# Kernel tuning notes

Measured on AMD Instinct MI355X. Metric: run time of the kernel, lower is better.

Reference implementation:

```python
import jax, jax.numpy as jnp
import numpy as np

EPS = 1e-6
T = 10.0
STEPS = 3
BN_EPS = 1e-5

def _normalize(x, axis):
    n = jnp.sqrt(jnp.sum(x * x, axis=axis, keepdims=True))
    return x / jnp.maximum(n, EPS)

def _vq_step(X, D):
    # X: (B, d, n), D: (B, d, r)
    Dn = _normalize(D, 1)
    Xn = _normalize(X, 1)
    cos = jnp.einsum('bdr,bdn->brn', Dn, Xn)          # (B, r, n)
    C = jax.nn.softmax(cos / T, axis=1)               # softmax over r
    XCt = jnp.einsum('bdn,brn->bdr', X, C)            # (B, d, r)
    sums = jnp.maximum(jnp.sum(C, axis=2), EPS)       # (B, r)
    D2 = _normalize(XCt / sums[:, None, :], 1)
    Xbar = jnp.einsum('bdr,brn->bdn', D2, C)
    return D2, C, Xbar

def _ham_vq(X, D0):
    # K-1 steps without gradient tracking, final step with grad through X only
    Xs = jax.lax.stop_gradient(X)
    def body(D, _):
        D, _, _ = _vq_step(Xs, D)
        return D, None
    D, _ = jax.lax.scan(body, _normalize(D0, 1), None, length=STEPS - 1)
    D = jax.lax.stop_gradient(D)
    _, _, Xbar = _vq_step(X, D)
    return Xbar

def _conv1x1(x, w, b=None):
    y = jnp.einsum('oc,bchw->bohw', w, x)
    if b is not None:
        y = y + b[None, :, None, None]
    return y

def _bn(x, gamma, beta, mean, var):
    inv = gamma / jnp.sqrt(var + BN_EPS)
    return x * inv[None, :, None, None] + (beta - mean * inv)[None, :, None, None]


def setup_inputs() -> dict:
    key = jax.random.key(0)
    ks = jax.random.split(key, 16)
    B, Cin, H, W = 8, 512, 64, 64
    d_mid, r = 512, 64
    out_ch = 2 * d_mid  # dual
    sc = 0.02
    inp = {
        'z': jax.random.normal(ks[0], (B, Cin, H, W), jnp.float32),
        'lower_w': jax.random.normal(ks[1], (out_ch, Cin), jnp.float32) * sc,
        'lower_b': jnp.zeros((out_ch,), jnp.float32),
        'Dinit_s': jax.random.uniform(ks[2], (B, d_mid, r), jnp.float32),
        'Dinit_c': jax.random.uniform(ks[3], (B, d_mid, r), jnp.float32),
        'cheese_w': jax.random.normal(ks[4], (out_ch, out_ch), jnp.float32) * sc,
        'ch_gamma': jnp.ones((out_ch,), jnp.float32),
        'ch_beta': jnp.zeros((out_ch,), jnp.float32),
        'ch_mean': jax.random.normal(ks[5], (out_ch,), jnp.float32) * 0.1,
        'ch_var': jax.random.uniform(ks[6], (out_ch,), jnp.float32) + 0.5,
        'upper_w': jax.random.normal(ks[7], (Cin, out_ch), jnp.float32) * sc,
        'upper_b': jnp.zeros((Cin,), jnp.float32),
        'h_gamma': jnp.ones((Cin,), jnp.float32),
        'h_beta': jnp.zeros((Cin,), jnp.float32),
        'h_mean': jax.random.normal(ks[8], (Cin,), jnp.float32) * 0.1,
        'h_var': jax.random.uniform(ks[9], (Cin,), jnp.float32) + 0.5,
        'coef_ham': jnp.array(1.0, jnp.float32),
        'coef_shortcut': jnp.array(1.0, jnp.float32),
    }
    return inp


def reference(z, lower_w, lower_b, Dinit_s, Dinit_c, cheese_w,
              ch_gamma, ch_beta, ch_mean, ch_var, upper_w, upper_b,
              h_gamma, h_beta, h_mean, h_var, coef_ham, coef_shortcut):
    B, Cin, H, W = z.shape
    identity = z
    # lower: conv1x1 + relu
    y = jax.nn.relu(_conv1x1(z, lower_w, lower_b))       # (B, 2*d_mid, H, W)
    d_mid = y.shape[1] // 2
    y1, y2 = y[:, :d_mid], y[:, d_mid:]
    n = H * W
    # spatial ham
    Xs = y1.reshape(B, d_mid, n)
    y1 = _ham_vq(Xs, Dinit_s).reshape(B, d_mid, H, W)
    # channel ham (same (B, d, n) flattening; HamMD requires dim1 == d_mid)
    Xc = y2.reshape(B, d_mid, n)
    y2 = _ham_vq(Xc, Dinit_c).reshape(B, d_mid, H, W)
    y = jnp.concatenate([y1, y2], axis=1)
    # cheese: conv1x1(no bias) + BN + relu
    y = jax.nn.relu(_bn(_conv1x1(y, cheese_w), ch_gamma, ch_beta, ch_mean, ch_var))
    # upper conv1x1 + BN
    h = _bn(_conv1x1(y, upper_w, upper_b), h_gamma, h_beta, h_mean, h_var)
    out = coef_ham * h + coef_shortcut * identity
    return jax.nn.relu(out)
```

## Files before the change

### kernel.cpp

```cpp
#include <hip/hip_runtime.h>
#include <hip/hip_bf16.h>

typedef __bf16 bf16_t;
typedef __bf16 bf16x4 __attribute__((ext_vector_type(4)));
typedef __bf16 bf16x8 __attribute__((ext_vector_type(8)));
typedef float  f32x4  __attribute__((ext_vector_type(4)));

#define HEPS 1e-6f

__device__ __forceinline__ void gload16(const bf16_t* g, bf16_t* l) {
    __builtin_amdgcn_global_load_lds(
        (const __attribute__((address_space(1))) unsigned int*)(g),
        (__attribute__((address_space(3))) unsigned int*)(l),
        16, 0, 0);
}


__global__ void cvt_f32_bf16_k(const float* __restrict__ src, bf16_t* __restrict__ dst, int n) {
    int i = blockIdx.x * 256 + threadIdx.x;
    if (i < n) dst[i] = (bf16_t)src[i];
}

__global__ void prep_k(const float* __restrict__ chg, const float* __restrict__ chb,
                       const float* __restrict__ chm, const float* __restrict__ chv,
                       const float* __restrict__ hg, const float* __restrict__ hb,
                       const float* __restrict__ hm, const float* __restrict__ hv,
                       const float* __restrict__ ub, const float* __restrict__ cham,
                       float* __restrict__ chA, float* __restrict__ chB,
                       float* __restrict__ hA2, float* __restrict__ hB2) {
    int i = blockIdx.x * 256 + threadIdx.x;
    if (i < 1024) {
        float inv = chg[i] * rsqrtf(chv[i] + 1e-5f);
        chA[i] = inv;
        chB[i] = chb[i] - chm[i] * inv;
    }
    if (i < 512) {
        float inv = hg[i] * rsqrtf(hv[i] + 1e-5f);
        float cA = cham[0];
        hA2[i] = cA * inv;
        hB2[i] = cA * (fmaf(ub[i], inv, hb[i]) - hm[i] * inv);
    }
}

__global__ void tz_k(const float* __restrict__ z, bf16_t* __restrict__ Zt) {
    __shared__ bf16_t t[64][68];
    int b = blockIdx.z, kt = blockIdx.y, nt = blockIdx.x;
    const float* src = z + ((size_t)b * 512 + kt * 64) * 4096 + nt * 64;
    int tid = threadIdx.x;
    int kr = tid >> 4;
    int nc = (tid & 15) * 4;
    #pragma unroll
    for (int it = 0; it < 4; ++it) {
        int k = kr + it * 16;
        float4 v = *(const float4*)&src[(size_t)k * 4096 + nc];
        t[nc + 0][k] = (bf16_t)v.x; t[nc + 1][k] = (bf16_t)v.y;
        t[nc + 2][k] = (bf16_t)v.z; t[nc + 3][k] = (bf16_t)v.w;
    }
    __syncthreads();
    bf16_t* dst = Zt + ((size_t)b * 4096 + nt * 64) * 512 + kt * 64;
    int nr = tid >> 4;
    int kc = (tid & 15) * 4;
    #pragma unroll
    for (int it = 0; it < 4; ++it) {
        int n = nr + it * 16;
        bf16x4 o;
        #pragma unroll
        for (int c = 0; c < 4; ++c) o[c] = t[n][kc + c];
        *(bf16x4*)&dst[(size_t)n * 512 + kc] = o;
    }
}

__global__ void dinit_k(const float* __restrict__ Ds, const float* __restrict__ Dc,
                        bf16_t* __restrict__ Dt) {
    int bs = blockIdx.y;
    int b = bs >> 1;
    const float* src = ((bs & 1) ? Dc : Ds) + (size_t)b * 512 * 64;
    int idx = blockIdx.x * 256 + threadIdx.x;
    int r = idx & 63, d = idx >> 6;
    Dt[(size_t)bs * 64 * 512 + (size_t)r * 512 + d] = (bf16_t)src[d * 64 + r];
}

__global__ void xnorm2_k(const bf16_t* __restrict__ Xt, float* __restrict__ xinv) {
    int gid = blockIdx.x * 4 + (threadIdx.x >> 6);
    int lane = threadIdx.x & 63;
    bf16x8 v = *(const bf16x8*)(Xt + (size_t)gid * 512 + lane * 8);
    float s = 0.f;
    #pragma unroll
    for (int e = 0; e < 8; ++e) { float f = (float)v[e]; s += f * f; }
    #pragma unroll
    for (int off = 32; off > 0; off >>= 1) s += __shfl_xor(s, off);
    if (lane == 0) xinv[gid] = 1.0f / (10.0f * fmaxf(sqrtf(s), HEPS));
}

__global__ void dnorm_k(const bf16_t* __restrict__ Dt, float* __restrict__ dinv) {
    int gw = (blockIdx.x * 256 + threadIdx.x) >> 6;
    int lane = threadIdx.x & 63;
    bf16x8 v = *(const bf16x8*)(Dt + (size_t)gw * 512 + lane * 8);
    float s = 0.f;
    #pragma unroll
    for (int e = 0; e < 8; ++e) { float f = (float)v[e]; s += f * f; }
    #pragma unroll
    for (int off = 32; off > 0; off >>= 1) s += __shfl_xor(s, off);
    if (lane == 0) dinv[gw] = 1.0f / fmaxf(sqrtf(s), HEPS);
}

__global__ void reduce_k(const float* __restrict__ P, bf16_t* __restrict__ Dt,
                         float* __restrict__ dinv) {
    int bsr = blockIdx.x;
    int bs = bsr >> 6, r = bsr & 63;
    int lane = threadIdx.x;
    const float* base = P + ((size_t)(bs * 4) * 64 + r) * 512 + lane * 8;
    float s[8] = {0.f, 0.f, 0.f, 0.f, 0.f, 0.f, 0.f, 0.f};
    #pragma unroll
    for (int kc = 0; kc < 4; ++kc) {
        const float* p = base + (size_t)kc * 64 * 512;
        float4 u = *(const float4*)p;
        float4 w = *(const float4*)(p + 4);
        s[0] += u.x; s[1] += u.y; s[2] += u.z; s[3] += u.w;
        s[4] += w.x; s[5] += w.y; s[6] += w.z; s[7] += w.w;
    }
    bf16x8 o;
    float sq = 0.f;
    #pragma unroll
    for (int e = 0; e < 8; ++e) { sq += s[e] * s[e]; o[e] = (bf16_t)s[e]; }
    *(bf16x8*)&Dt[(size_t)bsr * 512 + lane * 8] = o;
    #pragma unroll
    for (int off = 32; off > 0; off >>= 1) sq += __shfl_xor(sq, off);
    if (lane == 0) dinv[bsr] = 1.0f / fmaxf(sqrtf(sq), HEPS);
}

template<int BM, int BN, int WAVES_M, int WAVES_N, int EPI, int ORDER>
__launch_bounds__(256)
__global__ void g2(const bf16_t* __restrict__ Ag, const bf16_t* __restrict__ Bg,
                   void* __restrict__ Cg, void* __restrict__ C2g,
                   const int M, const int N, const int K,
                   const int ldA, const int ldB, const int ldC,
                   const long aStride, const long bStride,
                   const long cStride, const long c2Stride,
                   const float* __restrict__ p0, const float* __restrict__ p1,
                   const float* __restrict__ scal,
                   const float* __restrict__ shortcut, const long sStride)
{
    constexpr int WM = BM / WAVES_M, WN = BN / WAVES_N;
    constexpr int FM = WM / 16, FN = WN / 16;
    constexpr int ASEG = BM / 64, BSEG = BN / 64;
    constexpr int LPT = ASEG + BSEG;

    __shared__ __align__(64) bf16_t SH[3 * (BM + BN) * 32];
    __shared__ float dl[64];
    bf16_t* Al = SH;
    bf16_t* Bl = SH + 3 * BM * 32;

    const int tid = threadIdx.x;
    const int wave = tid >> 6, lane = tid & 63;
    const int l15 = lane & 15, q = lane >> 4;
    const int lrow = lane >> 2, lcol = (lane & 3) * 8;

    const int gx = gridDim.x, gy = gridDim.y;
    const int per = gx * gy;
    const int nwg = per * gridDim.z;
    const int g = blockIdx.z * per + blockIdx.y * gx + blockIdx.x;
    const int qq = nwg >> 3, rr = nwg & 7;
    const int xcd = g & 7, jj = g >> 3;
    const int w = (xcd < rr ? xcd * (qq + 1) : rr * (qq + 1) + (xcd - rr) * qq) + jj;
    const int bz = w / per;
    const int rem = w - bz * per;
    int bx, by;
    if constexpr (ORDER == 0) { by = rem / gx; bx = rem - by * gx; }
    else                      { bx = rem / gy; by = rem - bx * gy; }

    int bs = bz, exA = 0, exB = 0;
    if constexpr (EPI == 5) { bs = bz >> 2; exA = exB = (bz & 3) * 1024; }
    if constexpr (EPI == 7) { exA = (bz & 1) * 512; }

    const int n0 = bx * BN;
    const int m0 = by * BM;
    const int wm0 = (wave / WAVES_N) * WM;
    const int wn0 = (wave % WAVES_N) * WN;

    const bf16_t* Ab = Ag + (size_t)bs * (size_t)aStride + exA;
    const bf16_t* Bb = Bg + (size_t)bs * (size_t)bStride + exB;

    if constexpr (EPI == 6) { if (tid < 64) dl[tid] = p0[bz * 64 + tid]; }

    auto stage = [&](int buf, int k0) {
        #pragma unroll
        for (int t = 0; t < ASEG; ++t) {
            int seg = wave * ASEG + t;
            gload16(Ab + (size_t)(m0 + seg * 16 + lrow) * ldA + k0 + lcol,
                    &Al[buf * BM * 32 + seg * 512]);
        }
        #pragma unroll
        for (int t = 0; t < BSEG; ++t) {
            int seg = wave * BSEG + t;
            gload16(Bb + (size_t)(n0 + seg * 16 + lrow) * ldB + k0 + lcol,
                    &Bl[buf * BN * 32 + seg * 512]);
        }
    };

    f32x4 acc[FM][FN];
    #pragma unroll
    for (int i = 0; i < FM; ++i)
        #pragma unroll
        for (int j = 0; j < FN; ++j)
            #pragma unroll
            for (int e = 0; e < 4; ++e) acc[i][j][e] = 0.f;

    const int nK = K / 32;
    stage(0, 0);
    if (nK > 1) stage(1, 32);

    for (int t = 0; t < nK; ++t) {
        const int cur = t % 3;
        if (t + 2 < nK) stage((t + 2) % 3, (t + 2) * 32);

        const int ahead = (nK - 1 - t < 2) ? (nK - 1 - t) : 2;
        if (ahead == 2)      asm volatile("s_waitcnt vmcnt(%0)" :: "i"(2 * LPT) : "memory");
        else if (ahead == 1) asm volatile("s_waitcnt vmcnt(%0)" :: "i"(LPT) : "memory");
        else                 asm volatile("s_waitcnt vmcnt(0)" ::: "memory");
        __builtin_amdgcn_s_barrier();
        __builtin_amdgcn_sched_barrier(0);

        bf16x8 af[FM], bfm[FN];
        #pragma unroll
        for (int i = 0; i < FM; ++i)
            af[i] = *(const bf16x8*)&Al[cur * BM * 32 + (wm0 + 16 * i + l15) * 32 + 8 * q];
        #pragma unroll
        for (int j = 0; j < FN; ++j)
            bfm[j] = *(const bf16x8*)&Bl[cur * BN * 32 + (wn0 + 16 * j + l15) * 32 + 8 * q];

        __builtin_amdgcn_s_setprio(1);
        #pragma unroll
        for (int i = 0; i < FM; ++i)
            #pragma unroll
            for (int j = 0; j < FN; ++j)
                acc[i][j] = __builtin_amdgcn_mfma_f32_16x16x32_bf16(af[i], bfm[j], acc[i][j], 0, 0, 0);
        __builtin_amdgcn_s_setprio(0);

        __builtin_amdgcn_sched_barrier(0);
        __builtin_amdgcn_s_barrier();
    }

    int rowB[FM];
    #pragma unroll
    for (int i = 0; i < FM; ++i) rowB[i] = m0 + wm0 + 16 * i + 4 * q;
    const int colBase = n0 + wn0;

    if constexpr (EPI == 1) {
        constexpr int LP = 132;
        bf16_t* sp = SH;
        bf16_t* X  = (bf16_t*)Cg  + (size_t)bz * (size_t)cStride;
        bf16_t* Xt = (bf16_t*)C2g + (size_t)bz * (size_t)c2Stride;
        const int s = m0 >> 9, d0b = m0 & 511;
        __syncthreads();
        #pragma unroll
        for (int i = 0; i < FM; ++i) {
            int rl = wm0 + 16 * i + 4 * q;
            #pragma unroll
            for (int j = 0; j < FN; ++j) {
                int cl = wn0 + 16 * j + l15;
                #pragma unroll
                for (int e = 0; e < 4; ++e) {
                    float v = fmaxf(acc[i][j][e] + p0[m0 + rl + e], 0.f);
                    sp[(rl + e) * LP + cl] = (bf16_t)v;
                }
            }
        }
        __syncthreads();
        {
            int row = tid >> 1, cb = (tid & 1) * 64;
            #pragma unroll
            for (int u = 0; u < 8; ++u) {
                bf16x8 v = *(const bf16x8*)&sp[row * LP + cb + u * 8];
                *(bf16x8*)&X[(size_t)(m0 + row) * ldC + n0 + cb + u * 8] = v;
            }
        }
        __syncthreads();
        #pragma unroll
        for (int i = 0; i < FM; ++i) {
            int rl = wm0 + 16 * i + 4 * q;
            #pragma unroll
            for (int j = 0; j < FN; ++j) {
                int cl = wn0 + 16 * j + l15;
                #pragma unroll
                for (int e = 0; e < 4; ++e) {
                    float v = fmaxf(acc[i][j][e] + p0[m0 + rl + e], 0.f);
                    sp[cl * LP + rl + e] = (bf16_t)v;
                }
            }
        }
        __syncthreads();
        {
            int col = tid >> 1, db = (tid & 1) * 64;
            #pragma unroll
            for (int u = 0; u < 8; ++u) {
                bf16x8 v = *(const bf16x8*)&sp[col * LP + db + u * 8];
                *(bf16x8*)&Xt[((size_t)s * 4096 + n0 + col) * 512 + d0b + db + u * 8] = v;
            }
        }
    } else if constexpr (EPI == 2) {
        bf16_t* O = (bf16_t*)Cg + (size_t)bz * (size_t)cStride;
        #pragma unroll
        for (int j = 0; j < FN; ++j) {
            int col = colBase + 16 * j + l15;
            float a = p0[col], b = p1[col];
            #pragma unroll
            for (int i = 0; i < FM; ++i) {
                int rb = rowB[i];
                #pragma unroll
                for (int e = 0; e < 4; ++e) {
                    float v = fmaxf(fmaf(acc[i][j][e], a, b), 0.f);
                    O[(size_t)(rb + e) * ldC + col] = (bf16_t)v;
                }
            }
        }
    } else if constexpr (EPI == 3) {
        float* O = (float*)Cg + (size_t)bz * (size_t)cStride;
        const float* sc = shortcut + (size_t)bz * (size_t)sStride;
        float cB = scal[0];
        #pragma unroll
        for (int i = 0; i < FM; ++i) {
            int rb = rowB[i];
            #pragma unroll
            for (int e = 0; e < 4; ++e) {
                int row = rb + e;
                float a = p0[row], b = p1[row];
                #pragma unroll
                for (int j = 0; j < FN; ++j) {
                    int col = colBase + 16 * j + l15;
                    float v = fmaf(acc[i][j][e], a, b) + cB * sc[(size_t)row * ldC + col];
                    O[(size_t)row * ldC + col] = fmaxf(v, 0.f);
                }
            }
        }
    } else if constexpr (EPI == 5) {
        float* O = (float*)Cg + (size_t)bz * (size_t)cStride;
        #pragma unroll
        for (int i = 0; i < FM; ++i) {
            int rb = rowB[i];
            #pragma unroll
            for (int j = 0; j < FN; ++j) {
                int col = colBase + 16 * j + l15;
                *(f32x4*)&O[(size_t)col * ldC + rb] = acc[i][j];
            }
        }
    } else if constexpr (EPI == 6) {
        bf16_t* Cc = (bf16_t*)Cg  + (size_t)bz * (size_t)cStride;
        bf16_t* Ct = (bf16_t*)C2g + (size_t)(bz >> 1) * (size_t)c2Stride;
        const int hoff = (bz & 1) * 64;
        const bool doCt = (C2g != nullptr);
        #pragma unroll
        for (int j = 0; j < FN; ++j) {
            int col = colBase + 16 * j + l15;
            float xi = p1[bz * 4096 + col];
            float mx = -1e30f;
            #pragma unroll
            for (int i = 0; i < FM; ++i)
                #pragma unroll
                for (int e = 0; e < 4; ++e) {
                    float v = acc[i][j][e] * dl[rowB[i] + e] * xi;
                    acc[i][j][e] = v;
                    mx = fmaxf(mx, v);
                }
            mx = fmaxf(mx, __shfl_xor(mx, 16));
            mx = fmaxf(mx, __shfl_xor(mx, 32));
            float sm = 0.f;
            #pragma unroll
            for (int i = 0; i < FM; ++i)
                #pragma unroll
                for (int e = 0; e < 4; ++e) {
                    float p = __expf(acc[i][j][e] - mx);
                    acc[i][j][e] = p;
                    sm += p;
                }
            sm += __shfl_xor(sm, 16);
            sm += __shfl_xor(sm, 32);
            float rs = 1.0f / sm;
            #pragma unroll
            for (int i = 0; i < FM; ++i) {
                int rb = rowB[i];
                bf16x4 t;
                #pragma unroll
                for (int e = 0; e < 4; ++e) {
                    t[e] = (bf16_t)(acc[i][j][e] * rs);
                    Cc[(size_t)(rb + e) * ldC + col] = t[e];
                }
                if (doCt) *(bf16x4*)&Ct[(size_t)col * 128 + hoff + rb] = t;
            }
        }
    } else if constexpr (EPI == 7) {
        bf16_t* O = (bf16_t*)Cg + (size_t)(bz >> 1) * (size_t)cStride;
        const int hoff = (bz & 1) * 64;
        #pragma unroll
        for (int j = 0; j < FN; ++j) {
            int col = colBase + 16 * j + l15;
            float di = p0[bz * 64 + col];
            #pragma unroll
            for (int i = 0; i < FM; ++i) {
                int rb = rowB[i];
                #pragma unroll
                for (int e = 0; e < 4; ++e)
                    O[(size_t)(rb + e) * 128 + hoff + col] = (bf16_t)(acc[i][j][e] * di);
            }
        }
    }
}


extern "C" void kernel_launch(void* const* d_in, const int* in_sizes, int n_in,
                              void* d_out, int out_size, void* d_ws, size_t ws_size,
                              hipStream_t stream) {
    const float* z        = (const float*)d_in[0];
    const float* lower_w  = (const float*)d_in[1];
    const float* lower_b  = (const float*)d_in[2];
    const float* Dinit_s  = (const float*)d_in[3];
    const float* Dinit_c  = (const float*)d_in[4];
    const float* cheese_w = (const float*)d_in[5];
    const float* ch_gamma = (const float*)d_in[6];
    const float* ch_beta  = (const float*)d_in[7];
    const float* ch_mean  = (const float*)d_in[8];
    const float* ch_var   = (const float*)d_in[9];
    const float* upper_w  = (const float*)d_in[10];
    const float* upper_b  = (const float*)d_in[11];
    const float* h_gamma  = (const float*)d_in[12];
    const float* h_beta   = (const float*)d_in[13];
    const float* h_mean   = (const float*)d_in[14];
    const float* h_var    = (const float*)d_in[15];
    const float* coef_ham = (const float*)d_in[16];
    const float* coef_sc  = (const float*)d_in[17];

    char* ws = (char*)d_ws;
    size_t off = 0;
    auto alloc = [&](size_t bytes) -> void* {
        void* p = ws + off;
        off += (bytes + 255) & ~(size_t)255;
        return p;
    };

    bf16_t* Wl   = (bf16_t*)alloc((size_t)1024 * 512 * 2);
    bf16_t* Wc   = (bf16_t*)alloc((size_t)1024 * 1024 * 2);
    bf16_t* Wu   = (bf16_t*)alloc((size_t)512 * 1024 * 2);
    float*  chA  = (float*) alloc(1024 * 4);
    float*  chB  = (float*) alloc(1024 * 4);
    float*  hA2  = (float*) alloc(512 * 4);
    float*  hB2  = (float*) alloc(512 * 4);
    float*  dinv = (float*) alloc(1024 * 4);
    float*  xinv = (float*) alloc((size_t)16 * 4096 * 4);
    bf16_t* Xbf  = (bf16_t*)alloc((size_t)8 * 1024 * 4096 * 2);
    bf16_t* Xt   = (bf16_t*)alloc((size_t)16 * 4096 * 512 * 2);
    bf16_t* Zt   = (bf16_t*)alloc((size_t)8 * 4096 * 512 * 2);
    bf16_t* Cb   = (bf16_t*)alloc((size_t)16 * 64 * 4096 * 2);
    bf16_t* Ct2  = (bf16_t*)alloc((size_t)8 * 4096 * 128 * 2);
    float*  P    = (float*) alloc((size_t)64 * 64 * 512 * 4);
    bf16_t* Dta  = (bf16_t*)alloc((size_t)16 * 64 * 512 * 2);
    bf16_t* Dtb  = (bf16_t*)alloc((size_t)16 * 64 * 512 * 2);
    bf16_t* Eb   = (bf16_t*)alloc((size_t)8 * 1024 * 128 * 2);
    bf16_t* Ycht = Xbf;

    dim3 blk(256);

    cvt_f32_bf16_k<<<2048, blk, 0, stream>>>(lower_w, Wl, 1024 * 512);
    cvt_f32_bf16_k<<<4096, blk, 0, stream>>>(cheese_w, Wc, 1024 * 1024);
    cvt_f32_bf16_k<<<2048, blk, 0, stream>>>(upper_w, Wu, 512 * 1024);
    prep_k<<<4, blk, 0, stream>>>(ch_gamma, ch_beta, ch_mean, ch_var,
                                  h_gamma, h_beta, h_mean, h_var,
                                  upper_b, coef_ham, chA, chB, hA2, hB2);
    tz_k<<<dim3(64, 8, 8), blk, 0, stream>>>(z, Zt);
    dinit_k<<<dim3(128, 16), blk, 0, stream>>>(Dinit_s, Dinit_c, Dta);

    g2<128, 128, 2, 2, 1, 1><<<dim3(32, 8, 8), blk, 0, stream>>>(
        Wl, Zt, (void*)Xbf, (void*)Xt, 1024, 4096, 512,
        512, 512, 4096,
        0L, (long)4096 * 512, (long)1024 * 4096, (long)2 * 4096 * 512,
        lower_b, nullptr, nullptr, nullptr, 0L);

    xnorm2_k<<<16384, blk, 0, stream>>>(Xt, xinv);
    dnorm_k<<<256, blk, 0, stream>>>(Dta, dinv);

    bf16_t* cur = Dta;
    bf16_t* nxt = Dtb;
    for (int t = 0; t < 3; ++t) {
        g2<64, 256, 1, 4, 6, 0><<<dim3(16, 1, 16), blk, 0, stream>>>(
            cur, Xt, (void*)Cb, (t == 2) ? (void*)Ct2 : nullptr, 64, 4096, 512,
            512, 512, 4096,
            (long)64 * 512, (long)4096 * 512, (long)64 * 4096, (long)4096 * 128,
            dinv, xinv, nullptr, nullptr, 0L);
        g2<128, 64, 2, 2, 5, 0><<<dim3(1, 4, 64), blk, 0, stream>>>(
            Xbf, Cb, (void*)P, nullptr, 512, 64, 1024,
            4096, 4096, 512,
            (long)512 * 4096, (long)64 * 4096, (long)64 * 512, 0L,
            nullptr, nullptr, nullptr, nullptr, 0L);
        reduce_k<<<1024, dim3(64), 0, stream>>>(P, nxt, dinv);
        bf16_t* tmp = cur; cur = nxt; nxt = tmp;
    }

    g2<128, 64, 2, 2, 7, 0><<<dim3(1, 8, 16), blk, 0, stream>>>(
        Wc, cur, (void*)Eb, nullptr, 1024, 64, 512,
        1024, 512, 128,
        0L, (long)64 * 512, (long)1024 * 128, 0L,
        dinv, nullptr, nullptr, nullptr, 0L);

    g2<128, 128, 2, 2, 2, 0><<<dim3(8, 32, 8), blk, 0, stream>>>(
        Ct2, Eb, (void*)Ycht, nullptr, 4096, 1024, 128,
        128, 128, 1024,
        (long)4096 * 128, (long)1024 * 128, (long)4096 * 1024, 0L,
        chA, chB, nullptr, nullptr, 0L);

    g2<128, 128, 2, 2, 3, 1><<<dim3(32, 4, 8), blk, 0, stream>>>(
        Wu, Ycht, d_out, nullptr, 512, 4096, 1024,
        1024, 1024, 4096,
        0L, (long)4096 * 1024, (long)512 * 4096, 0L,
        hA2, hB2, coef_sc, z, (long)512 * 4096);

    (void)in_sizes; (void)n_in; (void)out_size; (void)ws_size;
}
```

Baseline: 345.9 us.

## Swap lower conv GEMM operands to emit position-major X directly

The lower 1x1 conv GEMM now computes the transposed product (positions × channels), so its natural output is the position-major Xt with 1024-wide rows. The channel-major Xbf copy is written with strided 4-element stores. This drops the LDS-staged double transpose epilogue and its extra barriers. The VQ GEMM and the norm kernel now index Xt with a doubled row stride and a half offset to select the spatial or channel half. The catch is that Xbf is written by scattered, less coalesced stores.

```diff
diff --git a/kernel.cpp b/kernel.cpp
--- a/kernel.cpp
+++ b/kernel.cpp
@@ -83,7 +83,9 @@
 __global__ void xnorm2_k(const bf16_t* __restrict__ Xt, float* __restrict__ xinv) {
     int gid = blockIdx.x * 4 + (threadIdx.x >> 6);
     int lane = threadIdx.x & 63;
-    bf16x8 v = *(const bf16x8*)(Xt + (size_t)gid * 512 + lane * 8);
+    int bs = gid >> 12, n = gid & 4095;
+    const bf16_t* row = Xt + ((size_t)(bs >> 1) * 4096 + n) * 1024 + (bs & 1) * 512 + lane * 8;
+    bf16x8 v = *(const bf16x8*)row;
     float s = 0.f;
     #pragma unroll
     for (int e = 0; e < 8; ++e) { float f = (float)v[e]; s += f * f; }
@@ -179,7 +181,11 @@
     const int wn0 = (wave % WAVES_N) * WN;
 
     const bf16_t* Ab = Ag + (size_t)bs * (size_t)aStride + exA;
-    const bf16_t* Bb = Bg + (size_t)bs * (size_t)bStride + exB;
+    const bf16_t* Bb;
+    if constexpr (EPI == 6)
+        Bb = Bg + (size_t)(bz >> 1) * (size_t)bStride + (size_t)(bz & 1) * 512;
+    else
+        Bb = Bg + (size_t)bs * (size_t)bStride + exB;
 
     if constexpr (EPI == 6) { if (tid < 64) dl[tid] = p0[bz * 64 + tid]; }
 
@@ -246,59 +252,7 @@
     for (int i = 0; i < FM; ++i) rowB[i] = m0 + wm0 + 16 * i + 4 * q;
     const int colBase = n0 + wn0;
 
-    if constexpr (EPI == 1) {
-        constexpr int LP = 132;
-        bf16_t* sp = SH;
-        bf16_t* X  = (bf16_t*)Cg  + (size_t)bz * (size_t)cStride;
-        bf16_t* Xt = (bf16_t*)C2g + (size_t)bz * (size_t)c2Stride;
-        const int s = m0 >> 9, d0b = m0 & 511;
-        __syncthreads();
-        #pragma unroll
-        for (int i = 0; i < FM; ++i) {
-            int rl = wm0 + 16 * i + 4 * q;
-            #pragma unroll
-            for (int j = 0; j < FN; ++j) {
-                int cl = wn0 + 16 * j + l15;
-                #pragma unroll
-                for (int e = 0; e < 4; ++e) {
-                    float v = fmaxf(acc[i][j][e] + p0[m0 + rl + e], 0.f);
-                    sp[(rl + e) * LP + cl] = (bf16_t)v;
-                }
-            }
-        }
-        __syncthreads();
-        {
-            int row = tid >> 1, cb = (tid & 1) * 64;
-            #pragma unroll
-            for (int u = 0; u < 8; ++u) {
-                bf16x8 v = *(const bf16x8*)&sp[row * LP + cb + u * 8];
-                *(bf16x8*)&X[(size_t)(m0 + row) * ldC + n0 + cb + u * 8] = v;
-            }
-        }
-        __syncthreads();
-        #pragma unroll
-        for (int i = 0; i < FM; ++i) {
-            int rl = wm0 + 16 * i + 4 * q;
-            #pragma unroll
-            for (int j = 0; j < FN; ++j) {
-                int cl = wn0 + 16 * j + l15;
-                #pragma unroll
-                for (int e = 0; e < 4; ++e) {
-                    float v = fmaxf(acc[i][j][e] + p0[m0 + rl + e], 0.f);
-                    sp[cl * LP + rl + e] = (bf16_t)v;
-                }
-            }
-        }
-        __syncthreads();
-        {
-            int col = tid >> 1, db = (tid & 1) * 64;
-            #pragma unroll
-            for (int u = 0; u < 8; ++u) {
-                bf16x8 v = *(const bf16x8*)&sp[col * LP + db + u * 8];
-                *(bf16x8*)&Xt[((size_t)s * 4096 + n0 + col) * 512 + d0b + db + u * 8] = v;
-            }
-        }
-    } else if constexpr (EPI == 2) {
+    if constexpr (EPI == 2) {
         bf16_t* O = (bf16_t*)Cg + (size_t)bz * (size_t)cStride;
         #pragma unroll
         for (int j = 0; j < FN; ++j) {
@@ -401,6 +355,26 @@
                 #pragma unroll
                 for (int e = 0; e < 4; ++e)
                     O[(size_t)(rb + e) * 128 + hoff + col] = (bf16_t)(acc[i][j][e] * di);
+            }
+        }
+    } else if constexpr (EPI == 8) {
+        bf16_t* O  = (bf16_t*)Cg  + (size_t)bz * (size_t)cStride;
+        bf16_t* O2 = (bf16_t*)C2g + (size_t)bz * (size_t)c2Stride;
+        #pragma unroll
+        for (int j = 0; j < FN; ++j) {
+            int col = colBase + 16 * j + l15;
+            float bias = p0[col];
+            #pragma unroll
+            for (int i = 0; i < FM; ++i) {
+                int rb = rowB[i];
+                bf16x4 t;
+                #pragma unroll
+                for (int e = 0; e < 4; ++e) {
+                    float v = fmaxf(acc[i][j][e] + bias, 0.f);
+                    t[e] = (bf16_t)v;
+                    O[(size_t)(rb + e) * ldC + col] = t[e];
+                }
+                *(bf16x4*)&O2[(size_t)col * 4096 + rb] = t;
             }
         }
     }
@@ -447,7 +421,7 @@
     float*  dinv = (float*) alloc(1024 * 4);
     float*  xinv = (float*) alloc((size_t)16 * 4096 * 4);
     bf16_t* Xbf  = (bf16_t*)alloc((size_t)8 * 1024 * 4096 * 2);
-    bf16_t* Xt   = (bf16_t*)alloc((size_t)16 * 4096 * 512 * 2);
+    bf16_t* Xt   = (bf16_t*)alloc((size_t)8 * 4096 * 1024 * 2);
     bf16_t* Zt   = (bf16_t*)alloc((size_t)8 * 4096 * 512 * 2);
     bf16_t* Cb   = (bf16_t*)alloc((size_t)16 * 64 * 4096 * 2);
     bf16_t* Ct2  = (bf16_t*)alloc((size_t)8 * 4096 * 128 * 2);
@@ -468,10 +442,10 @@
     tz_k<<<dim3(64, 8, 8), blk, 0, stream>>>(z, Zt);
     dinit_k<<<dim3(128, 16), blk, 0, stream>>>(Dinit_s, Dinit_c, Dta);
 
-    g2<128, 128, 2, 2, 1, 1><<<dim3(32, 8, 8), blk, 0, stream>>>(
-        Wl, Zt, (void*)Xbf, (void*)Xt, 1024, 4096, 512,
-        512, 512, 4096,
-        0L, (long)4096 * 512, (long)1024 * 4096, (long)2 * 4096 * 512,
+    g2<128, 128, 2, 2, 8, 0><<<dim3(8, 32, 8), blk, 0, stream>>>(
+        Zt, Wl, (void*)Xt, (void*)Xbf, 4096, 1024, 512,
+        512, 512, 1024,
+        (long)4096 * 512, 0L, (long)4096 * 1024, (long)1024 * 4096,
         lower_b, nullptr, nullptr, nullptr, 0L);
 
     xnorm2_k<<<16384, blk, 0, stream>>>(Xt, xinv);
@@ -482,8 +456,8 @@
     for (int t = 0; t < 3; ++t) {
         g2<64, 256, 1, 4, 6, 0><<<dim3(16, 1, 16), blk, 0, stream>>>(
             cur, Xt, (void*)Cb, (t == 2) ? (void*)Ct2 : nullptr, 64, 4096, 512,
-            512, 512, 4096,
-            (long)64 * 512, (long)4096 * 512, (long)64 * 4096, (long)4096 * 128,
+            512, 1024, 4096,
+            (long)64 * 512, (long)4096 * 1024, (long)64 * 4096, (long)4096 * 128,
             dinv, xinv, nullptr, nullptr, 0L);
         g2<128, 64, 2, 2, 5, 0><<<dim3(1, 4, 64), blk, 0, stream>>>(
             Xbf, Cb, (void*)P, nullptr, 512, 64, 1024,
```

Result: faster. 327.3 us (-5.4%).
